# Kernel optimization log

Hardware: AMD Instinct MI355X
Metric: run time of the kernel (lower is better)

Reference implementation:

```python
import jax, jax.numpy as jnp
import numpy as np

B, T, D, H = 2, 2048, 1024, 16
HD = D // H
FF = 4 * D
EPS = 1e-5


def rmsnorm(x, w):
    var = jnp.mean(jnp.square(x), axis=-1, keepdims=True)
    return x * jax.lax.rsqrt(var + EPS) * w


def setup_inputs() -> dict:
    key = jax.random.key(0)
    ks = jax.random.split(key, 17)
    sc = 0.02
    d = {}
    d["x"] = jax.random.normal(ks[0], (B, T, D), jnp.float32)
    d["x_token"] = jax.random.normal(ks[1], (B, T, D), jnp.float32)
    d["pos_emb"] = jax.random.normal(ks[2], (T, D), jnp.float32)
    d["lc_weight"] = jax.random.normal(ks[3], (1,), jnp.float32)
    d["Wq"] = jax.random.normal(ks[4], (D, D), jnp.float32) * sc  # per-head query weights stacked
    d["Wk"] = jax.random.normal(ks[5], (D, D), jnp.float32) * sc
    d["Wv"] = jax.random.normal(ks[6], (D, D), jnp.float32) * sc
    d["proj_w"] = jax.random.normal(ks[7], (D, D), jnp.float32) * sc
    d["proj_b"] = jnp.zeros((D,), jnp.float32)
    d["w1_w"] = jax.random.normal(ks[8], (FF, D), jnp.float32) * sc
    d["w1_b"] = jnp.zeros((FF,), jnp.float32)
    d["w2_w"] = jax.random.normal(ks[9], (D, FF), jnp.float32) * sc
    d["w2_b"] = jnp.zeros((D,), jnp.float32)
    d["w3_w"] = jax.random.normal(ks[10], (FF, D), jnp.float32) * sc
    d["w3_b"] = jnp.zeros((FF,), jnp.float32)
    d["norm1_w"] = jnp.ones((D,), jnp.float32)
    d["norm2_w"] = jnp.ones((D,), jnp.float32)
    return d


def reference(x, x_token, pos_emb, lc_weight, Wq, Wk, Wv, proj_w, proj_b,
              w1_w, w1_b, w2_w, w2_b, w3_w, w3_b, norm1_w, norm2_w):
    lc = jax.nn.sigmoid(lc_weight)  # scalar gate
    x_att = lc * x + (1.0 - lc) * x_token
    xn = rmsnorm(x_att, norm1_w)

    # q, v from normed gated input; k from raw positional embedding (faithful to source)
    q = (xn @ Wq.T).reshape(B, T, H, HD)
    k = (pos_emb @ Wk.T).reshape(T, H, HD)
    v = (xn @ Wv.T).reshape(B, T, H, HD)

    # NOTE: scale uses full model dim E (=D), not head_size, as in the source
    scores = jnp.einsum('bqhd,khd->bhqk', q, k) * (D ** -0.5)
    causal = jnp.tril(jnp.ones((T, T), bool))
    scores = jnp.where(causal, scores, -jnp.inf)
    p = jax.nn.softmax(scores, axis=-1)
    attn = jnp.einsum('bhqk,bkhd->bqhd', p, v).reshape(B, T, D)

    x = x + attn @ proj_w.T + proj_b

    xn2 = rmsnorm(x, norm2_w)
    h = jax.nn.silu(xn2 @ w1_w.T + w1_b) * (xn2 @ w3_w.T + w3_b)
    return x + h @ w2_w.T + w2_b
```

## Files before the change

### kernel.cpp

```cpp
#include <hip/hip_runtime.h>
#include <hip/hip_bf16.h>


typedef __hip_bfloat16 bf16;
typedef __attribute__((ext_vector_type(8))) short bf16x8;
typedef __attribute__((ext_vector_type(4))) float floatx4;

constexpr int cB = 2, cT = 2048, cD = 1024, cH = 16, cFF = 4096;
constexpr float cEPS = 1e-5f;
constexpr unsigned BF16_ONES = 0x3F803F80u;

__device__ __forceinline__ float b2f(bf16 x) { return __bfloat162float(x); }
__device__ __forceinline__ bf16  f2b(float x) { return __float2bfloat16(x); }
__device__ __forceinline__ unsigned short f2bu(float x) {
  bf16 t = __float2bfloat16(x);
  union { bf16 b; unsigned short u; } cv;
  cv.b = t;
  return cv.u;
}
__device__ __forceinline__ float loadR(const bf16* p)  { return b2f(*p); }
__device__ __forceinline__ float loadR(const float* p) { return *p; }

__device__ __forceinline__ void gload16(const bf16* g, unsigned short* l) {
  __builtin_amdgcn_global_load_lds(
      (const __attribute__((address_space(1))) void*)g,
      (__attribute__((address_space(3))) void*)l, 16, 0, 0);
}

__device__ __forceinline__ int xcd_remap1(int lin, int n) {
  return (lin & 7) * (n >> 3) + (lin >> 3);
}

struct ConvArgs {
  const void* src[17];
  bf16* dst[17];
  int n[17];
  int sb[17];
};

__global__ __launch_bounds__(256) void convert_all_k(ConvArgs a) {
  const int bid = blockIdx.x;
  int seg = 0;
#pragma unroll
  for (int i = 1; i < 17; i++) seg = (bid >= a.sb[i]) ? i : seg;
  const int n = a.n[seg];
  const int i0 = (bid - a.sb[seg]) * 2048 + threadIdx.x * 8;
  if (i0 >= n) return;
  const bool isb = (((const unsigned*)a.src[15])[0] == BF16_ONES);
  const void* src = a.src[seg];
  bf16* dst = a.dst[seg];
  if (i0 + 8 <= n) {
    if (isb) {
      *(int4*)(dst + i0) = *(const int4*)((const bf16*)src + i0);
    } else {
      float4 f0 = *(const float4*)((const float*)src + i0);
      float4 f1 = *(const float4*)((const float*)src + i0 + 4);
      int4 ro;
      bf16* po = (bf16*)&ro;
      po[0] = f2b(f0.x); po[1] = f2b(f0.y); po[2] = f2b(f0.z); po[3] = f2b(f0.w);
      po[4] = f2b(f1.x); po[5] = f2b(f1.y); po[6] = f2b(f1.z); po[7] = f2b(f1.w);
      *(int4*)(dst + i0) = ro;
    }
  } else {
    for (int j = i0; j < n; j++)
      dst[j] = isb ? ((const bf16*)src)[j] : f2b(((const float*)src)[j]);
  }
}

template <int OUTK, typename ResT>
__device__ __forceinline__ void gemm_core64(
    const bf16* __restrict__ A, const bf16* __restrict__ W,
    const bf16* __restrict__ bias, const ResT* __restrict__ R,
    void* __restrict__ Cv,
    int N, int Kst, int kb, int klen, int m0, int n0,
    unsigned short* As, unsigned short* Bs)
{
  const int tid  = threadIdx.x;
  const int wave = tid >> 6;
  const int lane = tid & 63;
  const int l15  = lane & 15;
  const int quad = lane >> 4;
  const int wm   = (wave >> 1) * 64;
  const int wn   = (wave & 1) * 32;

  const int lr  = lane >> 2;
  const int lc8 = (lane & 3) * 8;
  const bf16* Ag0 = A + (size_t)(m0 + wave * 32 + lr) * Kst + kb + lc8;
  const bf16* Ag1 = Ag0 + (size_t)16 * Kst;
  const bf16* Bg0 = W + (size_t)(n0 + wave * 16 + lr) * Kst + kb + lc8;
  unsigned short* lA0 = &As[(wave * 32) * 32];
  unsigned short* lA1 = &As[(wave * 32 + 16) * 32];
  unsigned short* lB0 = &Bs[(wave * 16) * 32];

  floatx4 acc[4][2];
#pragma unroll
  for (int i = 0; i < 4; i++)
#pragma unroll
    for (int j = 0; j < 2; j++) acc[i][j] = (floatx4){0.f, 0.f, 0.f, 0.f};

  for (int k0 = 0; k0 < klen; k0 += 64) {
    gload16(Ag0 + k0, lA0);
    gload16(Ag1 + k0, lA1);
    gload16(Ag0 + k0 + 32, lA0 + 128 * 32);
    gload16(Ag1 + k0 + 32, lA1 + 128 * 32);
    gload16(Bg0 + k0, lB0);
    gload16(Bg0 + k0 + 32, lB0 + 64 * 32);
    __syncthreads();

    bf16x8 a[4][2], b[2][2];
#pragma unroll
    for (int t = 0; t < 4; t++)
#pragma unroll
      for (int kh = 0; kh < 2; kh++)
        a[t][kh] = *(const bf16x8*)&As[kh * 128 * 32 + (wm + t * 16 + l15) * 32 + quad * 8];
#pragma unroll
    for (int u = 0; u < 2; u++)
#pragma unroll
      for (int kh = 0; kh < 2; kh++)
        b[u][kh] = *(const bf16x8*)&Bs[kh * 64 * 32 + (wn + u * 16 + l15) * 32 + quad * 8];
#pragma unroll
    for (int tm = 0; tm < 4; tm++)
#pragma unroll
      for (int tn = 0; tn < 2; tn++)
#pragma unroll
        for (int kh = 0; kh < 2; kh++)
          acc[tm][tn] = __builtin_amdgcn_mfma_f32_16x16x32_bf16(a[tm][kh], b[tn][kh], acc[tm][tn], 0, 0, 0);
    __syncthreads();
  }

#pragma unroll
  for (int tm = 0; tm < 4; tm++) {
#pragma unroll
    for (int tn = 0; tn < 2; tn++) {
      const int row = m0 + wm + tm * 16 + quad * 4;
      const int col = n0 + wn + tn * 16 + l15;
      float bv = (OUTK != 3 && bias) ? b2f(bias[col]) : 0.f;
#pragma unroll
      for (int i = 0; i < 4; i++) {
        float val = acc[tm][tn][i] + bv;
        const size_t cidx = (size_t)(row + i) * N + col;
        if (OUTK == 3) {
          atomicAdd((float*)Cv + cidx, val);
        } else if (OUTK == 4) {
          ((bf16*)Cv)[(size_t)col * (size_t)(cB * cT) + (row + i)] = f2b(val);
        } else {
          if (R) val += loadR(&R[cidx]);
          if (OUTK == 0) ((bf16*)Cv)[cidx] = f2b(val);
          else           ((float*)Cv)[cidx] = val;
        }
      }
    }
  }
}

template <int OUTK, typename ResT>
__global__ __launch_bounds__(256) void gemm_f(
    const bf16* __restrict__ A, const bf16* __restrict__ W,
    const bf16* __restrict__ bias, const ResT* __restrict__ R,
    void* __restrict__ Cv, int N, int Kst, int kchunk, int gx, int gxy)
{
  __shared__ __align__(16) unsigned short As[2 * 128 * 32];
  __shared__ __align__(16) unsigned short Bs[2 * 64 * 32];
  const int lin = xcd_remap1(blockIdx.x, gridDim.x);
  const int kz  = lin / gxy;
  const int rem = lin % gxy;
  gemm_core64<OUTK, ResT>(A, W, bias, R, Cv, N, Kst, kz * kchunk, kchunk,
                          (rem / gx) * 128, (rem % gx) * 64, As, Bs);
}

__global__ __launch_bounds__(256) void gemm_qkv(
    const bf16* __restrict__ xn, const bf16* __restrict__ pos,
    const bf16* __restrict__ Wq, const bf16* __restrict__ Wv,
    const bf16* __restrict__ Wk,
    bf16* __restrict__ q, bf16* __restrict__ vT, bf16* __restrict__ kb)
{
  __shared__ __align__(16) unsigned short As[2 * 128 * 32];
  __shared__ __align__(16) unsigned short Bs[2 * 64 * 32];
  const int lin = xcd_remap1(blockIdx.x, gridDim.x);
  int z, local;
  if (lin < 512)       { z = 0; local = lin; }
  else if (lin < 1024) { z = 1; local = lin - 512; }
  else                 { z = 2; local = lin - 1024; }
  const int gx = 16;
  const int by = local / gx, bx = local % gx;
  if (z == 1) {
    gemm_core64<4, bf16>(xn, Wv, nullptr, (const bf16*)nullptr, vT,
                         cD, cD, 0, cD, by * 128, bx * 64, As, Bs);
  } else {
    const bf16* A = (z == 2) ? pos : xn;
    const bf16* W = (z == 0) ? Wq : Wk;
    bf16* C = (z == 0) ? q : kb;
    gemm_core64<0, bf16>(A, W, nullptr, (const bf16*)nullptr, C,
                         cD, cD, 0, cD, by * 128, bx * 64, As, Bs);
  }
}

__global__ __launch_bounds__(512, 2) void gemm8pf(
    const bf16* __restrict__ A,
    const bf16* __restrict__ W1, const bf16* __restrict__ b1,
    const bf16* __restrict__ W3, const bf16* __restrict__ b3,
    bf16* __restrict__ H)
{
  __shared__ __align__(16) unsigned short As[2 * 2 * 256 * 32];
  __shared__ __align__(16) unsigned short B1s[2 * 2 * 128 * 32];
  __shared__ __align__(16) unsigned short B3s[2 * 2 * 128 * 32];
  constexpr int K = cD;
  constexpr int NT = K / 64;
  const int lin = xcd_remap1(blockIdx.x, gridDim.x);
  const int by = lin & 15;
  const int bx = lin >> 4;
  const int m0 = by * 256, n0 = bx * 128;

  const int tid  = threadIdx.x;
  const int wave = tid >> 6;
  const int lane = tid & 63;
  const int l15  = lane & 15;
  const int quad = lane >> 4;
  const int wm   = wave >> 2;
  const int wq   = wave & 3;
  const int swz  = (quad ^ (l15 & 3) ^ ((l15 >> 2) & 3)) * 8;

  const int srowA = wave * 32 + (lane >> 2);
  const int sblk  = (lane & 3) ^ ((lane >> 2) & 3) ^ ((lane >> 4) & 3);
  const bf16* Ags = A + (size_t)(m0 + srowA) * K + sblk * 8;
  const int srowB = wave * 16 + (lane >> 2);
  const bf16* W1gs = W1 + (size_t)(n0 + srowB) * K + sblk * 8;
  const bf16* W3gs = W3 + (size_t)(n0 + srowB) * K + sblk * 8;
  unsigned short* const lA  = &As[0]  + (wave * 32) * 32;
  unsigned short* const lB1 = &B1s[0] + (wave * 16) * 32;
  unsigned short* const lB3 = &B3s[0] + (wave * 16) * 32;

  floatx4 acc1[8][2], acc3[8][2];
#pragma unroll
  for (int i = 0; i < 8; i++)
#pragma unroll
    for (int j = 0; j < 2; j++) {
      acc1[i][j] = (floatx4){0.f, 0.f, 0.f, 0.f};
      acc3[i][j] = (floatx4){0.f, 0.f, 0.f, 0.f};
    }

#define STAGE_A8(buf, kel, kh)                                              \
  { const bf16* s_ = Ags + (kel) + (kh) * 32;                               \
    unsigned short* d_ = lA + (buf) * (2 * 256 * 32) + (kh) * (256 * 32);   \
    gload16(s_, d_);                                                        \
    gload16(s_ + (size_t)16 * K, d_ + 16 * 32); }
#define STAGE_B8(buf, kel, kh)                                              \
  { gload16(W1gs + (kel) + (kh) * 32,                                       \
            lB1 + (buf) * (2 * 128 * 32) + (kh) * (128 * 32));              \
    gload16(W3gs + (kel) + (kh) * 32,                                       \
            lB3 + (buf) * (2 * 128 * 32) + (kh) * (128 * 32)); }

#define WAITBAR4()                                                          \
  asm volatile("s_waitcnt vmcnt(4)" ::: "memory");                          \
  __builtin_amdgcn_sched_barrier(0);                                        \
  __builtin_amdgcn_s_barrier();                                             \
  __builtin_amdgcn_sched_barrier(0);

  STAGE_A8(0, 0, 0); STAGE_B8(0, 0, 0); STAGE_A8(0, 0, 1); STAGE_B8(0, 0, 1);
  asm volatile("s_waitcnt vmcnt(0)" ::: "memory");
  __builtin_amdgcn_sched_barrier(0);
  __builtin_amdgcn_s_barrier();
  __builtin_amdgcn_sched_barrier(0);

  int buf = 0;
#pragma unroll 1
  for (int t = 0; t < NT; ++t) {
    const int nkel = (t + 1) * 64;
    const bool pf = (t + 1 < NT);
    const unsigned short* ab  = &As[0]  + buf * (2 * 256 * 32);
    const unsigned short* bb1 = &B1s[0] + buf * (2 * 128 * 32);
    const unsigned short* bb3 = &B3s[0] + buf * (2 * 128 * 32);
    bf16x8 bf1[2], bf3[2], af[4];

    WAITBAR4();
#pragma unroll
    for (int nf = 0; nf < 2; nf++) {
      bf1[nf] = *(const bf16x8*)&bb1[(wq * 32 + nf * 16 + l15) * 32 + swz];
      bf3[nf] = *(const bf16x8*)&bb3[(wq * 32 + nf * 16 + l15) * 32 + swz];
    }
#pragma unroll
    for (int j = 0; j < 4; j++)
      af[j] = *(const bf16x8*)&ab[(wm * 128 + j * 16 + l15) * 32 + swz];
    __builtin_amdgcn_sched_barrier(0);
    if (pf) STAGE_A8(buf ^ 1, nkel, 0);
    __builtin_amdgcn_s_setprio(1);
#pragma unroll
    for (int j = 0; j < 4; j++)
#pragma unroll
      for (int nf = 0; nf < 2; nf++) {
        acc1[j][nf] = __builtin_amdgcn_mfma_f32_16x16x32_bf16(af[j], bf1[nf], acc1[j][nf], 0, 0, 0);
        acc3[j][nf] = __builtin_amdgcn_mfma_f32_16x16x32_bf16(af[j], bf3[nf], acc3[j][nf], 0, 0, 0);
      }
    __builtin_amdgcn_s_setprio(0);

#pragma unroll
    for (int j = 0; j < 4; j++)
      af[j] = *(const bf16x8*)&ab[(wm * 128 + 64 + j * 16 + l15) * 32 + swz];
    __builtin_amdgcn_sched_barrier(0);
    if (pf) STAGE_B8(buf ^ 1, nkel, 0);
    __builtin_amdgcn_s_setprio(1);
#pragma unroll
    for (int j = 0; j < 4; j++)
#pragma unroll
      for (int nf = 0; nf < 2; nf++) {
        acc1[4 + j][nf] = __builtin_amdgcn_mfma_f32_16x16x32_bf16(af[j], bf1[nf], acc1[4 + j][nf], 0, 0, 0);
        acc3[4 + j][nf] = __builtin_amdgcn_mfma_f32_16x16x32_bf16(af[j], bf3[nf], acc3[4 + j][nf], 0, 0, 0);
      }
    __builtin_amdgcn_s_setprio(0);

    WAITBAR4();
#pragma unroll
    for (int nf = 0; nf < 2; nf++) {
      bf1[nf] = *(const bf16x8*)&bb1[128 * 32 + (wq * 32 + nf * 16 + l15) * 32 + swz];
      bf3[nf] = *(const bf16x8*)&bb3[128 * 32 + (wq * 32 + nf * 16 + l15) * 32 + swz];
    }
#pragma unroll
    for (int j = 0; j < 4; j++)
      af[j] = *(const bf16x8*)&ab[256 * 32 + (wm * 128 + j * 16 + l15) * 32 + swz];
    __builtin_amdgcn_sched_barrier(0);
    if (pf) STAGE_A8(buf ^ 1, nkel, 1);
    __builtin_amdgcn_s_setprio(1);
#pragma unroll
    for (int j = 0; j < 4; j++)
#pragma unroll
      for (int nf = 0; nf < 2; nf++) {
        acc1[j][nf] = __builtin_amdgcn_mfma_f32_16x16x32_bf16(af[j], bf1[nf], acc1[j][nf], 0, 0, 0);
        acc3[j][nf] = __builtin_amdgcn_mfma_f32_16x16x32_bf16(af[j], bf3[nf], acc3[j][nf], 0, 0, 0);
      }
    __builtin_amdgcn_s_setprio(0);

#pragma unroll
    for (int j = 0; j < 4; j++)
      af[j] = *(const bf16x8*)&ab[256 * 32 + (wm * 128 + 64 + j * 16 + l15) * 32 + swz];
    __builtin_amdgcn_sched_barrier(0);
    if (pf) STAGE_B8(buf ^ 1, nkel, 1);
    __builtin_amdgcn_s_setprio(1);
#pragma unroll
    for (int j = 0; j < 4; j++)
#pragma unroll
      for (int nf = 0; nf < 2; nf++) {
        acc1[4 + j][nf] = __builtin_amdgcn_mfma_f32_16x16x32_bf16(af[j], bf1[nf], acc1[4 + j][nf], 0, 0, 0);
        acc3[4 + j][nf] = __builtin_amdgcn_mfma_f32_16x16x32_bf16(af[j], bf3[nf], acc3[4 + j][nf], 0, 0, 0);
      }
    __builtin_amdgcn_s_setprio(0);

    buf ^= 1;
  }
#undef STAGE_A8
#undef STAGE_B8
#undef WAITBAR4

#pragma unroll
  for (int mf = 0; mf < 8; mf++) {
#pragma unroll
    for (int nf = 0; nf < 2; nf++) {
      const int row = m0 + wm * 128 + mf * 16 + quad * 4;
      const int col = n0 + wq * 32 + nf * 16 + l15;
      const float bv1 = b2f(b1[col]);
      const float bv3 = b2f(b3[col]);
#pragma unroll
      for (int i = 0; i < 4; i++) {
        float g = acc1[mf][nf][i] + bv1;
        float u = acc3[mf][nf][i] + bv3;
        float v = g * (1.f / (1.f + __expf(-g))) * u;
        H[(size_t)(row + i) * cFF + col] = f2b(v);
      }
    }
  }
}

template <bool GATE, typename InT>
__global__ __launch_bounds__(256) void rmsnorm_k(
    const InT* __restrict__ X, const bf16* __restrict__ XT,
    const bf16* __restrict__ LC, const bf16* __restrict__ Wn,
    bf16* __restrict__ O, float* __restrict__ Z)
{
  const int row = blockIdx.x;
  const int tid = threadIdx.x;
  const size_t base = (size_t)row * cD;
  const int c = tid * 4;

  if (Z) *(float4*)(Z + base + c) = (float4){0.f, 0.f, 0.f, 0.f};

  float lc = 1.f, lc1 = 0.f;
  if (GATE) {
    float g = b2f(LC[0]);
    lc = 1.f / (1.f + __expf(-g));
    lc1 = 1.f - lc;
  }

  float xv[4];
  if (sizeof(InT) == 2) {
    ushort4 u = *(const ushort4*)((const unsigned short*)X + base + c);
    const bf16* pu = (const bf16*)&u;
#pragma unroll
    for (int i = 0; i < 4; i++) xv[i] = b2f(pu[i]);
  } else {
    float4 f = *(const float4*)((const float*)X + base + c);
    xv[0] = f.x; xv[1] = f.y; xv[2] = f.z; xv[3] = f.w;
  }
  if (GATE) {
    ushort4 u = *(const ushort4*)((const unsigned short*)XT + base + c);
    const bf16* pu = (const bf16*)&u;
#pragma unroll
    for (int i = 0; i < 4; i++) xv[i] = lc * xv[i] + lc1 * b2f(pu[i]);
  }

  float ss = xv[0] * xv[0] + xv[1] * xv[1] + xv[2] * xv[2] + xv[3] * xv[3];
#pragma unroll
  for (int off = 32; off; off >>= 1) ss += __shfl_xor(ss, off, 64);

  __shared__ float red[4];
  if ((tid & 63) == 0) red[tid >> 6] = ss;
  __syncthreads();
  float tot = red[0] + red[1] + red[2] + red[3];
  float rs = rsqrtf(tot * (1.f / cD) + cEPS);

  ushort4 o;
  bf16* po = (bf16*)&o;
#pragma unroll
  for (int i = 0; i < 4; i++) po[i] = f2b(xv[i] * rs * b2f(Wn[c + i]));
  *(ushort4*)((unsigned short*)O + base + c) = o;
}

__global__ __launch_bounds__(256) void combine_k(
    const float* __restrict__ P, const float* __restrict__ X2,
    const bf16* __restrict__ bias, void* __restrict__ out,
    const unsigned* __restrict__ dbits)
{
  const bool obf = (*dbits == BF16_ONES);
  const size_t idx = ((size_t)blockIdx.x * 256 + threadIdx.x) * 4;
  float4 p = *(const float4*)(P + idx);
  float4 x = *(const float4*)(X2 + idx);
  const int col = (int)(idx & (cD - 1));
  ushort4 bu = *(const ushort4*)((const unsigned short*)bias + col);
  const bf16* bb = (const bf16*)&bu;
  float v0 = p.x + x.x + b2f(bb[0]);
  float v1 = p.y + x.y + b2f(bb[1]);
  float v2 = p.z + x.z + b2f(bb[2]);
  float v3 = p.w + x.w + b2f(bb[3]);
  if (obf) {
    ushort4 o;
    bf16* po = (bf16*)&o;
    po[0] = f2b(v0); po[1] = f2b(v1); po[2] = f2b(v2); po[3] = f2b(v3);
    *(ushort4*)((unsigned short*)out + idx) = o;
  } else {
    *(float4*)((float*)out + idx) = (float4){v0, v1, v2, v3};
  }
}

__global__ __launch_bounds__(256) void fattn_k(
    const bf16* __restrict__ Q, const bf16* __restrict__ K,
    const bf16* __restrict__ Vt, bf16* __restrict__ O)
{
  constexpr int LQ = 72;
  constexpr int BT = cB * cT;
  __shared__ __align__(16) unsigned short Qs[64 * LQ];
  __shared__ __align__(16) unsigned short Ks[2 * 64 * 64];
  __shared__ __align__(16) unsigned short Vs[2 * 64 * 64];

  const int tid  = threadIdx.x;
  const int wave = tid >> 6;
  const int lane = tid & 63;
  const int l15  = lane & 15;
  const int quad = lane >> 4;
  const int blk  = xcd_remap1(blockIdx.x, gridDim.x);
  const int qt   = 31 - (blk & 31);
  const int h    = (blk >> 5) & 15;
  const int b    = blk >> 9;
  const int q0   = qt * 64;

  const bf16* Qb = Q + ((size_t)b * cT) * cD + h * 64;
  const bf16* Kb = K + h * 64;
  const bf16* Vb = Vt + (size_t)(h * 64) * BT + (size_t)b * cT;

  const int sr = lane >> 3;
  const int sc = ((lane & 7) ^ sr) * 8;
  unsigned short* const kd = &Ks[0] + wave * 512;
  unsigned short* const vd = &Vs[0] + wave * 512;

  auto STAGE = [&](int bf, int k0) {
    const bf16* ks = Kb + (size_t)(k0 + wave * 8 + sr) * cD + sc;
    gload16(ks,           kd + bf * 4096);
    gload16(ks + 32 * cD, kd + bf * 4096 + 2048);
    const bf16* vs = Vb + (size_t)(wave * 8 + sr) * BT + k0 + sc;
    gload16(vs,                   vd + bf * 4096);
    gload16(vs + (size_t)32 * BT, vd + bf * 4096 + 2048);
  };

  const int ktiles = qt + 1;
  STAGE(0, 0);

  {
    const int qr = tid >> 2, qc = (tid & 3) * 16;
    const bf16* gq = Qb + (size_t)(q0 + qr) * cD + qc;
    *(int4*)&Qs[qr * LQ + qc]     = *(const int4*)(gq);
    *(int4*)&Qs[qr * LQ + qc + 8] = *(const int4*)(gq + 8);
  }
  __syncthreads();

  const int qw = wave * 16;
  bf16x8 qa[2];
#pragma unroll
  for (int dc = 0; dc < 2; dc++)
    qa[dc] = *(const bf16x8*)&Qs[(qw + l15) * LQ + dc * 32 + quad * 8];

  float l_p[4] = {0.f, 0.f, 0.f, 0.f};
  floatx4 oacc[4];
#pragma unroll
  for (int dt = 0; dt < 4; dt++) oacc[dt] = (floatx4){0.f, 0.f, 0.f, 0.f};

  unsigned short* Pw = &Qs[qw * LQ];
  const int swk = l15 & 7;
  const int rb0 = (quad ^ swk) * 8;
  const int rb1 = ((quad + 4) ^ swk) * 8;

  int bf = 0;
  for (int it = 0; it < ktiles; ++it) {
    const int k0 = it * 64;
    if (it + 1 < ktiles) STAGE(bf ^ 1, k0 + 64);

    const unsigned short* kb_ = &Ks[bf * 4096];
    const unsigned short* vb_ = &Vs[bf * 4096];

    floatx4 s[4];
#pragma unroll
    for (int st = 0; st < 4; st++) {
      bf16x8 kb0 = *(const bf16x8*)&kb_[(st * 16 + l15) * 64 + rb0];
      bf16x8 kb1 = *(const bf16x8*)&kb_[(st * 16 + l15) * 64 + rb1];
      s[st] = (floatx4){0.f, 0.f, 0.f, 0.f};
      s[st] = __builtin_amdgcn_mfma_f32_16x16x32_bf16(qa[0], kb0, s[st], 0, 0, 0);
      s[st] = __builtin_amdgcn_mfma_f32_16x16x32_bf16(qa[1], kb1, s[st], 0, 0, 0);
    }
    float p[4][4];
#pragma unroll
    for (int i = 0; i < 4; i++) {
      const int qrow = q0 + qw + quad * 4 + i;
#pragma unroll
      for (int st = 0; st < 4; st++) {
        const int kp = k0 + st * 16 + l15;
        float pv = (kp > qrow) ? 0.f : __expf(s[st][i] * 0.03125f);
        p[st][i] = pv;
        l_p[i] += pv;
      }
    }
#pragma unroll
    for (int st = 0; st < 4; st++)
#pragma unroll
      for (int i = 0; i < 4; i++)
        Pw[(quad * 4 + i) * LQ + st * 16 + l15] = f2bu(p[st][i]);
    bf16x8 pa[2];
#pragma unroll
    for (int pc = 0; pc < 2; pc++)
      pa[pc] = *(const bf16x8*)&Pw[l15 * LQ + pc * 32 + quad * 8];
#pragma unroll
    for (int dt = 0; dt < 4; dt++) {
      bf16x8 vb0 = *(const bf16x8*)&vb_[(dt * 16 + l15) * 64 + rb0];
      bf16x8 vb1 = *(const bf16x8*)&vb_[(dt * 16 + l15) * 64 + rb1];
      oacc[dt] = __builtin_amdgcn_mfma_f32_16x16x32_bf16(pa[0], vb0, oacc[dt], 0, 0, 0);
      oacc[dt] = __builtin_amdgcn_mfma_f32_16x16x32_bf16(pa[1], vb1, oacc[dt], 0, 0, 0);
    }

    __syncthreads();
    bf ^= 1;
  }

  float rl[4];
#pragma unroll
  for (int i = 0; i < 4; i++) {
    float li = l_p[i];
#pragma unroll
    for (int off = 1; off < 16; off <<= 1) li += __shfl_xor(li, off, 64);
    rl[i] = 1.f / li;
  }
  const size_t obase = ((size_t)b * cT + q0 + qw) * cD + h * 64;
#pragma unroll
  for (int dt = 0; dt < 4; dt++)
#pragma unroll
    for (int i = 0; i < 4; i++)
      O[obase + (size_t)(quad * 4 + i) * cD + dt * 16 + l15] = f2b(oacc[dt][i] * rl[i]);
}

extern "C" void kernel_launch(void* const* d_in, const int* in_sizes, int n_in,
                              void* d_out, int out_size, void* d_ws, size_t ws_size,
                              hipStream_t stream) {
  char* ws = (char*)d_ws;
  const size_t MB = 1u << 20;
  const int BT = cB * cT;

  bf16* cxt  = (bf16*)(ws + 0);
  bf16* cpos = (bf16*)(ws + 8 * MB);
  bf16* q    = (bf16*)(ws + 12 * MB);
  bf16* kbuf = (bf16*)(ws + 20 * MB);
  bf16* vT   = (bf16*)(ws + 24 * MB);
  bf16* h    = (bf16*)(ws + 0);
  size_t off = 32 * MB;
  auto alloc = [&](size_t bytes) -> char* {
    char* p = ws + off;
    off = (off + bytes + 255) & ~(size_t)255;
    return p;
  };
  bf16*  cx  = (bf16*)alloc((size_t)BT * cD * 2);
  bf16*  xn  = (bf16*)alloc((size_t)BT * cD * 2);
  float* x2  = (float*)alloc((size_t)BT * cD * 4);
  bf16*  xn2 = (bf16*)alloc((size_t)BT * cD * 2);
  float* part = (float*)(ws + 32 * MB);
  bf16* cin[17];
  cin[0] = cx; cin[1] = cxt; cin[2] = cpos;
  for (int i = 3; i < 17; i++) cin[i] = (bf16*)alloc((size_t)in_sizes[i] * 2);

  const unsigned* dbits = (const unsigned*)d_in[15];
  dim3 blk(256);

  ConvArgs ca;
  int nblk = 0;
  for (int i = 0; i < 17; i++) {
    ca.src[i] = d_in[i];
    ca.dst[i] = cin[i];
    ca.n[i] = in_sizes[i];
    ca.sb[i] = nblk;
    nblk += (in_sizes[i] + 2047) / 2048;
  }
  convert_all_k<<<nblk, blk, 0, stream>>>(ca);

  const bf16 *clc = cin[3], *cWq = cin[4], *cWk = cin[5], *cWv = cin[6];
  const bf16 *cprojw = cin[7], *cprojb = cin[8];
  const bf16 *cw1w = cin[9], *cw1b = cin[10], *cw2w = cin[11], *cw2b = cin[12];
  const bf16 *cw3w = cin[13], *cw3b = cin[14], *cn1 = cin[15], *cn2 = cin[16];

  rmsnorm_k<true, bf16><<<BT, blk, 0, stream>>>(cx, cxt, clc, cn1, xn, nullptr);
  gemm_qkv<<<1280, blk, 0, stream>>>(xn, cpos, cWq, cWv, cWk, q, vT, kbuf);
  bf16* attn = xn;
  fattn_k<<<cB * cH * (cT / 64), blk, 0, stream>>>(q, kbuf, vT, attn);
  gemm_f<1, bf16><<<512, blk, 0, stream>>>(
      attn, cprojw, cprojb, cx, x2, cD, cD, cD, 16, 512);
  rmsnorm_k<false, float><<<BT, blk, 0, stream>>>(
      x2, (const bf16*)nullptr, (const bf16*)nullptr, cn2, xn2, part);
  gemm8pf<<<512, 512, 0, stream>>>(xn2, cw1w, cw1b, cw3w, cw3b, h);
  gemm_f<3, float><<<1024, blk, 0, stream>>>(
      h, cw2w, nullptr, (const float*)nullptr, part, cD, cFF, 2048, 16, 512);
  combine_k<<<BT, blk, 0, stream>>>(part, x2, cw2b, d_out, dbits);
  (void)n_in; (void)out_size; (void)ws_size;
}
```

Measured before the change: 428.4 us.

## Move QKV and W2 GEMMs onto 256x128 pipelined 8-wave GEMM core

Adds a generic 512-thread GEMM core with 256x128 tiles, double-buffered direct-to-LDS loads and staged prefetch, modeled on the existing fused W1/W3 kernel. The QKV projection and the split-K W2 GEMM (now four K-chunks of 1024 instead of two of 2048, still combined by atomic adds) are switched to it. The aim is more data reuse per tile and better overlap of loads with MFMA work. The final iteration now waits for all outstanding loads. The trade-off is fewer, larger blocks (320 for QKV), which may not fill all CUs evenly, and more atomic traffic for W2.

```diff
diff --git a/kernel.cpp b/kernel.cpp
--- a/kernel.cpp
+++ b/kernel.cpp
@@ -30,6 +30,12 @@
 __device__ __forceinline__ int xcd_remap1(int lin, int n) {
   return (lin & 7) * (n >> 3) + (lin >> 3);
 }
+
+#define WAITBAR_N(N)                                                        \
+  asm volatile("s_waitcnt vmcnt(" #N ")" ::: "memory");                     \
+  __builtin_amdgcn_sched_barrier(0);                                        \
+  __builtin_amdgcn_s_barrier();                                             \
+  __builtin_amdgcn_sched_barrier(0);
 
 struct ConvArgs {
   const void* src[17];
@@ -134,20 +140,14 @@
     for (int tn = 0; tn < 2; tn++) {
       const int row = m0 + wm + tm * 16 + quad * 4;
       const int col = n0 + wn + tn * 16 + l15;
-      float bv = (OUTK != 3 && bias) ? b2f(bias[col]) : 0.f;
+      float bv = bias ? b2f(bias[col]) : 0.f;
 #pragma unroll
       for (int i = 0; i < 4; i++) {
         float val = acc[tm][tn][i] + bv;
         const size_t cidx = (size_t)(row + i) * N + col;
-        if (OUTK == 3) {
-          atomicAdd((float*)Cv + cidx, val);
-        } else if (OUTK == 4) {
-          ((bf16*)Cv)[(size_t)col * (size_t)(cB * cT) + (row + i)] = f2b(val);
-        } else {
-          if (R) val += loadR(&R[cidx]);
-          if (OUTK == 0) ((bf16*)Cv)[cidx] = f2b(val);
-          else           ((float*)Cv)[cidx] = val;
-        }
+        if (R) val += loadR(&R[cidx]);
+        if (OUTK == 0) ((bf16*)Cv)[cidx] = f2b(val);
+        else           ((float*)Cv)[cidx] = val;
       }
     }
   }
@@ -168,31 +168,178 @@
                           (rem / gx) * 128, (rem % gx) * 64, As, Bs);
 }
 
-__global__ __launch_bounds__(256) void gemm_qkv(
+template <int OUTK>
+__device__ __forceinline__ void gemm8s_core(
+    const bf16* __restrict__ A, const bf16* __restrict__ W,
+    void* __restrict__ Cv, int N, int Kst, int kb, int NT, int m0, int n0,
+    unsigned short* As, unsigned short* Bs)
+{
+  const int tid  = threadIdx.x;
+  const int wave = tid >> 6;
+  const int lane = tid & 63;
+  const int l15  = lane & 15;
+  const int quad = lane >> 4;
+  const int wm   = wave >> 2;
+  const int wq   = wave & 3;
+  const int swz  = (quad ^ (l15 & 3) ^ ((l15 >> 2) & 3)) * 8;
+
+  const int srowA = wave * 32 + (lane >> 2);
+  const int sblk  = (lane & 3) ^ ((lane >> 2) & 3) ^ ((lane >> 4) & 3);
+  const bf16* Ags = A + (size_t)(m0 + srowA) * Kst + kb + sblk * 8;
+  const int srowB = wave * 16 + (lane >> 2);
+  const bf16* Wgs = W + (size_t)(n0 + srowB) * Kst + kb + sblk * 8;
+  unsigned short* const lA = As + (wave * 32) * 32;
+  unsigned short* const lB = Bs + (wave * 16) * 32;
+
+  floatx4 acc[8][2];
+#pragma unroll
+  for (int i = 0; i < 8; i++)
+#pragma unroll
+    for (int j = 0; j < 2; j++) acc[i][j] = (floatx4){0.f, 0.f, 0.f, 0.f};
+
+  auto S_A = [&](int buf, int kel, int kh) {
+    const bf16* s_ = Ags + kel + kh * 32;
+    unsigned short* d_ = lA + buf * (2 * 256 * 32) + kh * (256 * 32);
+    gload16(s_, d_);
+    gload16(s_ + (size_t)16 * Kst, d_ + 16 * 32);
+  };
+  auto S_B = [&](int buf, int kel, int kh) {
+    gload16(Wgs + kel + kh * 32, lB + buf * (2 * 128 * 32) + kh * (128 * 32));
+  };
+
+  S_A(0, 0, 0); S_B(0, 0, 0); S_A(0, 0, 1); S_B(0, 0, 1);
+  asm volatile("s_waitcnt vmcnt(0)" ::: "memory");
+  __builtin_amdgcn_sched_barrier(0);
+  __builtin_amdgcn_s_barrier();
+  __builtin_amdgcn_sched_barrier(0);
+
+  int buf = 0;
+#pragma unroll 1
+  for (int t = 0; t < NT; ++t) {
+    const int nkel = (t + 1) * 64;
+    const bool pf = (t + 1 < NT);
+    const unsigned short* ab = As + buf * (2 * 256 * 32);
+    const unsigned short* bb = Bs + buf * (2 * 128 * 32);
+    bf16x8 bfr[2], af[4];
+
+    WAITBAR_N(3)
+#pragma unroll
+    for (int nf = 0; nf < 2; nf++)
+      bfr[nf] = *(const bf16x8*)&bb[(wq * 32 + nf * 16 + l15) * 32 + swz];
+#pragma unroll
+    for (int j = 0; j < 4; j++)
+      af[j] = *(const bf16x8*)&ab[(wm * 128 + j * 16 + l15) * 32 + swz];
+    __builtin_amdgcn_sched_barrier(0);
+    if (pf) S_A(buf ^ 1, nkel, 0);
+    __builtin_amdgcn_s_setprio(1);
+#pragma unroll
+    for (int j = 0; j < 4; j++)
+#pragma unroll
+      for (int nf = 0; nf < 2; nf++)
+        acc[j][nf] = __builtin_amdgcn_mfma_f32_16x16x32_bf16(af[j], bfr[nf], acc[j][nf], 0, 0, 0);
+    __builtin_amdgcn_s_setprio(0);
+
+#pragma unroll
+    for (int j = 0; j < 4; j++)
+      af[j] = *(const bf16x8*)&ab[(wm * 128 + 64 + j * 16 + l15) * 32 + swz];
+    __builtin_amdgcn_sched_barrier(0);
+    if (pf) S_B(buf ^ 1, nkel, 0);
+    __builtin_amdgcn_s_setprio(1);
+#pragma unroll
+    for (int j = 0; j < 4; j++)
+#pragma unroll
+      for (int nf = 0; nf < 2; nf++)
+        acc[4 + j][nf] = __builtin_amdgcn_mfma_f32_16x16x32_bf16(af[j], bfr[nf], acc[4 + j][nf], 0, 0, 0);
+    __builtin_amdgcn_s_setprio(0);
+
+    if (pf) { WAITBAR_N(3) } else { WAITBAR_N(0) }
+#pragma unroll
+    for (int nf = 0; nf < 2; nf++)
+      bfr[nf] = *(const bf16x8*)&bb[128 * 32 + (wq * 32 + nf * 16 + l15) * 32 + swz];
+#pragma unroll
+    for (int j = 0; j < 4; j++)
+      af[j] = *(const bf16x8*)&ab[256 * 32 + (wm * 128 + j * 16 + l15) * 32 + swz];
+    __builtin_amdgcn_sched_barrier(0);
+    if (pf) S_A(buf ^ 1, nkel, 1);
+    __builtin_amdgcn_s_setprio(1);
+#pragma unroll
+    for (int j = 0; j < 4; j++)
+#pragma unroll
+      for (int nf = 0; nf < 2; nf++)
+        acc[j][nf] = __builtin_amdgcn_mfma_f32_16x16x32_bf16(af[j], bfr[nf], acc[j][nf], 0, 0, 0);
+    __builtin_amdgcn_s_setprio(0);
+
+#pragma unroll
+    for (int j = 0; j < 4; j++)
+      af[j] = *(const bf16x8*)&ab[256 * 32 + (wm * 128 + 64 + j * 16 + l15) * 32 + swz];
+    __builtin_amdgcn_sched_barrier(0);
+    if (pf) S_B(buf ^ 1, nkel, 1);
+    __builtin_amdgcn_s_setprio(1);
+#pragma unroll
+    for (int j = 0; j < 4; j++)
+#pragma unroll
+      for (int nf = 0; nf < 2; nf++)
+        acc[4 + j][nf] = __builtin_amdgcn_mfma_f32_16x16x32_bf16(af[j], bfr[nf], acc[4 + j][nf], 0, 0, 0);
+    __builtin_amdgcn_s_setprio(0);
+
+    buf ^= 1;
+  }
+
+#pragma unroll
+  for (int mf = 0; mf < 8; mf++) {
+#pragma unroll
+    for (int nf = 0; nf < 2; nf++) {
+      const int row = m0 + wm * 128 + mf * 16 + quad * 4;
+      const int col = n0 + wq * 32 + nf * 16 + l15;
+#pragma unroll
+      for (int i = 0; i < 4; i++) {
+        const float val = acc[mf][nf][i];
+        if (OUTK == 0) {
+          ((bf16*)Cv)[(size_t)(row + i) * N + col] = f2b(val);
+        } else if (OUTK == 4) {
+          ((bf16*)Cv)[(size_t)col * (size_t)(cB * cT) + (row + i)] = f2b(val);
+        } else {
+          atomicAdd((float*)Cv + (size_t)(row + i) * N + col, val);
+        }
+      }
+    }
+  }
+}
+
+__global__ __launch_bounds__(512, 2) void gemm_qkv8(
     const bf16* __restrict__ xn, const bf16* __restrict__ pos,
     const bf16* __restrict__ Wq, const bf16* __restrict__ Wv,
     const bf16* __restrict__ Wk,
     bf16* __restrict__ q, bf16* __restrict__ vT, bf16* __restrict__ kb)
 {
-  __shared__ __align__(16) unsigned short As[2 * 128 * 32];
-  __shared__ __align__(16) unsigned short Bs[2 * 64 * 32];
+  __shared__ __align__(16) unsigned short As[2 * 2 * 256 * 32];
+  __shared__ __align__(16) unsigned short Bs[2 * 2 * 128 * 32];
   const int lin = xcd_remap1(blockIdx.x, gridDim.x);
-  int z, local;
-  if (lin < 512)       { z = 0; local = lin; }
-  else if (lin < 1024) { z = 1; local = lin - 512; }
-  else                 { z = 2; local = lin - 1024; }
-  const int gx = 16;
-  const int by = local / gx, bx = local % gx;
-  if (z == 1) {
-    gemm_core64<4, bf16>(xn, Wv, nullptr, (const bf16*)nullptr, vT,
-                         cD, cD, 0, cD, by * 128, bx * 64, As, Bs);
+  if (lin < 128) {
+    gemm8s_core<0>(xn, Wq, q, cD, cD, 0, 16,
+                   (lin & 15) * 256, (lin >> 4) * 128, As, Bs);
+  } else if (lin < 256) {
+    const int l = lin - 128;
+    gemm8s_core<4>(xn, Wv, vT, cD, cD, 0, 16,
+                   (l & 15) * 256, (l >> 4) * 128, As, Bs);
   } else {
-    const bf16* A = (z == 2) ? pos : xn;
-    const bf16* W = (z == 0) ? Wq : Wk;
-    bf16* C = (z == 0) ? q : kb;
-    gemm_core64<0, bf16>(A, W, nullptr, (const bf16*)nullptr, C,
-                         cD, cD, 0, cD, by * 128, bx * 64, As, Bs);
-  }
+    const int l = lin - 256;
+    gemm8s_core<0>(pos, Wk, kb, cD, cD, 0, 16,
+                   (l & 7) * 256, (l >> 3) * 128, As, Bs);
+  }
+}
+
+__global__ __launch_bounds__(512, 2) void gemm_w2_8(
+    const bf16* __restrict__ H, const bf16* __restrict__ W2,
+    float* __restrict__ part)
+{
+  __shared__ __align__(16) unsigned short As[2 * 2 * 256 * 32];
+  __shared__ __align__(16) unsigned short Bs[2 * 2 * 128 * 32];
+  const int lin = xcd_remap1(blockIdx.x, gridDim.x);
+  const int kz  = lin >> 7;
+  const int rem = lin & 127;
+  gemm8s_core<3>(H, W2, part, cD, cFF, kz * 1024, 16,
+                 (rem & 15) * 256, (rem >> 4) * 128, As, Bs);
 }
 
 __global__ __launch_bounds__(512, 2) void gemm8pf(
@@ -250,12 +397,6 @@
     gload16(W3gs + (kel) + (kh) * 32,                                       \
             lB3 + (buf) * (2 * 128 * 32) + (kh) * (128 * 32)); }
 
-#define WAITBAR4()                                                          \
-  asm volatile("s_waitcnt vmcnt(4)" ::: "memory");                          \
-  __builtin_amdgcn_sched_barrier(0);                                        \
-  __builtin_amdgcn_s_barrier();                                             \
-  __builtin_amdgcn_sched_barrier(0);
-
   STAGE_A8(0, 0, 0); STAGE_B8(0, 0, 0); STAGE_A8(0, 0, 1); STAGE_B8(0, 0, 1);
   asm volatile("s_waitcnt vmcnt(0)" ::: "memory");
   __builtin_amdgcn_sched_barrier(0);
@@ -272,7 +413,7 @@
     const unsigned short* bb3 = &B3s[0] + buf * (2 * 128 * 32);
     bf16x8 bf1[2], bf3[2], af[4];
 
-    WAITBAR4();
+    WAITBAR_N(4)
 #pragma unroll
     for (int nf = 0; nf < 2; nf++) {
       bf1[nf] = *(const bf16x8*)&bb1[(wq * 32 + nf * 16 + l15) * 32 + swz];
@@ -308,7 +449,7 @@
       }
     __builtin_amdgcn_s_setprio(0);
 
-    WAITBAR4();
+    if (pf) { WAITBAR_N(4) } else { WAITBAR_N(0) }
 #pragma unroll
     for (int nf = 0; nf < 2; nf++) {
       bf1[nf] = *(const bf16x8*)&bb1[128 * 32 + (wq * 32 + nf * 16 + l15) * 32 + swz];
@@ -348,7 +489,6 @@
   }
 #undef STAGE_A8
 #undef STAGE_B8
-#undef WAITBAR4
 
 #pragma unroll
   for (int mf = 0; mf < 8; mf++) {
@@ -629,7 +769,7 @@
   const bf16 *cw3w = cin[13], *cw3b = cin[14], *cn1 = cin[15], *cn2 = cin[16];
 
   rmsnorm_k<true, bf16><<<BT, blk, 0, stream>>>(cx, cxt, clc, cn1, xn, nullptr);
-  gemm_qkv<<<1280, blk, 0, stream>>>(xn, cpos, cWq, cWv, cWk, q, vT, kbuf);
+  gemm_qkv8<<<320, 512, 0, stream>>>(xn, cpos, cWq, cWv, cWk, q, vT, kbuf);
   bf16* attn = xn;
   fattn_k<<<cB * cH * (cT / 64), blk, 0, stream>>>(q, kbuf, vT, attn);
   gemm_f<1, bf16><<<512, blk, 0, stream>>>(
@@ -637,8 +777,7 @@
   rmsnorm_k<false, float><<<BT, blk, 0, stream>>>(
       x2, (const bf16*)nullptr, (const bf16*)nullptr, cn2, xn2, part);
   gemm8pf<<<512, 512, 0, stream>>>(xn2, cw1w, cw1b, cw3w, cw3b, h);
-  gemm_f<3, float><<<1024, blk, 0, stream>>>(
-      h, cw2w, nullptr, (const float*)nullptr, part, cD, cFF, 2048, 16, 512);
+  gemm_w2_8<<<512, 512, 0, stream>>>(h, cw2w, part);
   combine_k<<<BT, blk, 0, stream>>>(part, x2, cw2b, d_out, dbits);
   (void)n_in; (void)out_size; (void)ws_size;
 }
```

New measurement: 491.0 us. 1.15x slower.
